# Kernel tuning notes

Hardware: AMD Instinct MI355X
Metric: run time of the kernel (lower is better)

The kernel has to match this reference:

```python
import jax, jax.numpy as jnp
from jax import lax
import numpy as np

KS = 3          # kernel_size
PAD = 1         # padding of conv_offset
N = KS * KS     # sampling points per pixel
B, C, H, W = 8, 64, 96, 96
OUTC = 64


def setup_inputs() -> dict:
    key = jax.random.key(0)
    k1, k2, k3 = jax.random.split(key, 3)
    x = jax.random.normal(k1, (B, C, H, W), dtype=jnp.float32)
    # conv_offset: Conv2d(C, 2N, ks=3, pad=1); small init so offsets are modest
    w_off = jax.random.normal(k2, (2 * N, C, KS, KS), dtype=jnp.float32) * 0.01
    b_off = jnp.zeros((2 * N,), jnp.float32)
    # conv_kernel: Conv2d(C, OUTC, ks=3, stride=3)
    w_ker = jax.random.normal(k3, (OUTC, C, KS, KS), dtype=jnp.float32) * (1.0 / np.sqrt(C * KS * KS))
    b_ker = jnp.zeros((OUTC,), jnp.float32)
    return {"x": x, "w_off": w_off, "b_off": b_off, "w_ker": w_ker, "b_ker": b_ker}


def _deform_conv(x, w_off, b_off, w_ker, b_ker):
    b, c, h, w = x.shape
    dn = ('NCHW', 'OIHW', 'NCHW')
    # offset field: (b, 2N, h, w); channels [:N] are x(row) offsets, [N:] are y(col)
    offset = lax.conv_general_dilated(x, w_off, (1, 1), [(PAD, PAD), (PAD, PAD)],
                                      dimension_numbers=dn) + b_off[None, :, None, None]
    r = jnp.arange(-(KS - 1) // 2, (KS - 1) // 2 + 1)
    pnx, pny = jnp.meshgrid(r, r, indexing='ij')          # kernel grid offsets p_n
    gx, gy = jnp.meshgrid(jnp.arange(h), jnp.arange(w), indexing='ij')  # p_0
    px = gx[None, None].astype(x.dtype) + pnx.reshape(1, N, 1, 1).astype(x.dtype) + offset[:, :N]
    py = gy[None, None].astype(x.dtype) + pny.reshape(1, N, 1, 1).astype(x.dtype) + offset[:, N:]
    # Bilinear sampling with zero outside the grid. This is exactly the dense
    # G @ x of the original (only the 4 neighbors of p have nonzero G weight).
    x0 = jnp.floor(px); y0 = jnp.floor(py)
    lx = px - x0; ly = py - y0            # grads flow to offsets through lx/ly
    x0i = lax.stop_gradient(x0).astype(jnp.int32)
    y0i = lax.stop_gradient(y0).astype(jnp.int32)
    x_flat = x.transpose(0, 2, 3, 1).reshape(b, h * w, c)  # (b, HW, c)

    def corner(xi, yi, wt):
        valid = ((xi >= 0) & (xi < h) & (yi >= 0) & (yi < w)).astype(x.dtype)
        idx = (jnp.clip(xi, 0, h - 1) * w + jnp.clip(yi, 0, w - 1)).reshape(b, -1)
        g = jax.vmap(lambda im, ix: im[ix])(x_flat, idx)   # (b, N*h*w, c)
        return g * (wt * valid).reshape(b, -1, 1)

    val = (corner(x0i,     y0i,     (1 - lx) * (1 - ly))
           + corner(x0i + 1, y0i,     lx * (1 - ly))
           + corner(x0i,     y0i + 1, (1 - lx) * ly)
           + corner(x0i + 1, y0i + 1, lx * ly))            # (b, N*h*w, c)
    xo = val.reshape(b, N, h, w, c).transpose(0, 4, 2, 3, 1)        # (b,c,h,w,N)
    # _reshape_x_offset: N -> (kr,kc) tiled into (h*ks, w*ks)
    xo = xo.reshape(b, c, h, w, KS, KS).transpose(0, 1, 2, 4, 3, 5).reshape(b, c, h * KS, w * KS)
    out = lax.conv_general_dilated(xo, w_ker, (KS, KS), 'VALID',
                                   dimension_numbers=dn) + b_ker[None, :, None, None]
    return out  # (b, OUTC, h, w)


def reference(x, w_off, b_off, w_ker, b_ker):
    return _deform_conv(x, w_off, b_off, w_ker, b_ker)
```

## Files before the change

kernel.cpp:

```cpp
#include <hip/hip_runtime.h>

#define H_ 96
#define W_ 96
#define HW 9216
#define C_ 64
#define OUTC 64
#define NPTS 9
#define NCH 18
#define B_ 8

#define PCH 72

typedef __attribute__((ext_vector_type(8))) short short8;
typedef __attribute__((ext_vector_type(4))) float f32x4;
typedef __attribute__((ext_vector_type(4))) unsigned int uint4v;

__device__ __forceinline__ short f2bf(float f) {
    union { float f; unsigned u; } v; v.f = f;
    unsigned r = v.u + 0x7fffu + ((v.u >> 16) & 1u);
    return (short)(r >> 16);
}
__device__ __forceinline__ float bflo(unsigned d) {
    union { unsigned u; float f; } v; v.u = d << 16; return v.f;
}
__device__ __forceinline__ float bfhi(unsigned d) {
    union { unsigned u; float f; } v; v.u = d & 0xffff0000u; return v.f;
}

__global__ __launch_bounds__(256) void prep_xpose(
    const float* __restrict__ x, const float* __restrict__ w_ker,
    const float* __restrict__ w_off, short* __restrict__ x_t,
    short* __restrict__ wk_frag, short* __restrict__ woff_frag)
{
    int blk = blockIdx.x;
    int t   = threadIdx.x;
    if (blk < 576) {
        int b   = blk & 7;
        int sub = blk >> 3;
        int cb  = t & 7;
        int px  = sub * 128 + (t >> 3) * 4;

        const float* xp = x + ((size_t)(b * C_ + cb * 8) * HW) + px;
        f32x4 tl[8];
#pragma unroll
        for (int e = 0; e < 8; ++e) tl[e] = *(const f32x4*)(xp + (size_t)e * HW);
#pragma unroll
        for (int p = 0; p < 4; ++p) {
            short8 s;
#pragma unroll
            for (int e = 0; e < 8; ++e) s[e] = f2bf(tl[e][p]);
            *(short8*)(x_t + ((size_t)(b * HW + px + p) * 64) + cb * 8) = s;
        }
    } else {
        int idx = (blk - 576) * 256 + t;
        if (idx < 36864) {
            int j = idx & 7, l = (idx >> 3) & 63, nt = (idx >> 9) & 3, sg = idx >> 11;
            int q2 = sg & 1, n = sg >> 1;
            int c  = q2 * 32 + ((l >> 4) << 3) + j;
            int oc = nt * 16 + (l & 15);
            wk_frag[idx] = f2bf(w_ker[(oc * C_ + c) * 9 + n]);
        } else {
            int k = idx - 36864;
            int j = k & 7, l = (k >> 3) & 63, nt = (k >> 9) & 1, sg = k >> 10;
            int q2 = sg & 1, n = sg >> 1;
            int c  = q2 * 32 + ((l >> 4) << 3) + j;
            int oc = nt * 16 + (l & 15);
            woff_frag[k] = (oc < NCH) ? f2bf(w_off[(oc * C_ + c) * 9 + n]) : (short)0;
        }
    }
}

__global__ __launch_bounds__(256, 5) void deform_fused(
    const short* __restrict__ x_t, const short* __restrict__ woff_frag,
    const float* __restrict__ b_off, const short* __restrict__ wk_frag,
    const float* __restrict__ b_ker, float* __restrict__ out)
{
    __shared__ __align__(16) short sX[160 * PCH];
    __shared__ float2 sP[4][16][9];

    int t    = threadIdx.x;
    int lane = t & 63;
    int wv   = t >> 6;
    int b    = blockIdx.x & 7;
    int s    = blockIdx.x >> 3;
    int rg   = s / 6;
    int cs   = s - rg * 6;
    int i0   = rg * 4;
    int j0   = cs * 16;
    int pxl  = lane & 15, kq = lane >> 4;
    int iw   = i0 + wv;
    int j    = j0 + pxl;
    const short* xb = x_t + (size_t)b * HW * 64;
    const short8 Z8 = {0,0,0,0,0,0,0,0};

#pragma unroll
    for (int k = 0; k < 5; ++k) {
        int u  = t + k * 256;
        int cb = u & 7, rc = u >> 3;
        int r = rc / 20, c = rc - r * 20;
        int row = min(max(i0 - 2 + r, 0), H_ - 1);
        int col = min(max(j0 - 2 + c, 0), W_ - 1);
        *(short8*)&sX[rc * PCH + cb * 8] =
            *(const short8*)(xb + (row * W_ + col) * 64 + cb * 8);
    }
    __syncthreads();

    f32x4 pa0 = {0,0,0,0}, pa1 = {0,0,0,0};
#pragma unroll
    for (int n = 0; n < 9; ++n) {
        int di = n / 3 - 1, dj = n % 3 - 1;
        bool ok = ((unsigned)(iw + di) < (unsigned)H_) & ((unsigned)(j + dj) < (unsigned)W_);
        int rcb = ((wv + di + 2) * 20 + (pxl + dj + 2)) * PCH;
#pragma unroll
        for (int q2 = 0; q2 < 2; ++q2) {
            short8 a = *(const short8*)&sX[rcb + q2 * 32 + kq * 8];
            a = ok ? a : Z8;
            const short* wb = woff_frag + ((n * 2 + q2) * 2) * 512 + lane * 8;
            short8 b0 = *(const short8*)(wb);
            short8 b1 = *(const short8*)(wb + 512);
            pa0 = __builtin_amdgcn_mfma_f32_16x16x32_bf16(a, b0, pa0, 0, 0, 0);
            pa1 = __builtin_amdgcn_mfma_f32_16x16x32_bf16(a, b1, pa1, 0, 0, 0);
        }
    }
    {
        int col = lane & 15, rq = lane >> 4;
        float bo = b_off[col];
        if (col < 9) {
#pragma unroll
            for (int r = 0; r < 4; ++r) sP[wv][rq * 4 + r][col].x = pa0[r] + bo;
        } else {
#pragma unroll
            for (int r = 0; r < 4; ++r) sP[wv][rq * 4 + r][col - 9].y = pa0[r] + bo;
        }
        if (col < 2) {
            float bo2 = b_off[16 + col];
#pragma unroll
            for (int r = 0; r < 4; ++r) sP[wv][rq * 4 + r][7 + col].y = pa1[r] + bo2;
        }
    }

    f32x4 acc[4];
#pragma unroll
    for (int nt = 0; nt < 4; ++nt) acc[nt] = (f32x4){0.f, 0.f, 0.f, 0.f};

#pragma unroll
    for (int n = 0; n < 9; ++n) {
        int di = n / 3 - 1, dj = n % 3 - 1;
        float2 o = sP[wv][pxl][n];
        float fpx = (float)(iw + di) + o.x;
        float fpy = (float)(j + dj) + o.y;
        float x0f = floorf(fpx), y0f = floorf(fpy);
        float lx = fpx - x0f, ly = fpy - y0f;
        int xi = (int)x0f, yi = (int)y0f;
        float wx0 = (xi >= 0  && xi <= H_ - 1) ? (1.0f - lx) : 0.0f;
        float wx1 = (xi >= -1 && xi <= H_ - 2) ? lx          : 0.0f;
        float wy0 = (yi >= 0  && yi <= W_ - 1) ? (1.0f - ly) : 0.0f;
        float wy1 = (yi >= -1 && yi <= W_ - 2) ? ly          : 0.0f;
        float w00 = wx0 * wy0, w10 = wx1 * wy0, w01 = wx0 * wy1, w11 = wx1 * wy1;
        int rp = xi - (i0 - 2), cp = yi - (j0 - 2);
        bool inp = (rp >= 0) & (rp <= 6) & (cp >= 0) & (cp <= 18);
        uint4v u[8];
        if (inp) {
            int l00 = (rp * 20 + cp) * PCH;
            int l10 = l00 + 20 * PCH, l01 = l00 + PCH, l11 = l10 + PCH;
#pragma unroll
            for (int q2 = 0; q2 < 2; ++q2) {
                int cho = q2 * 32 + kq * 8;
                u[q2*4+0] = *(const uint4v*)&sX[l00 + cho];
                u[q2*4+1] = *(const uint4v*)&sX[l10 + cho];
                u[q2*4+2] = *(const uint4v*)&sX[l01 + cho];
                u[q2*4+3] = *(const uint4v*)&sX[l11 + cho];
            }
        }
        if (!inp) {
            int r0 = min(max(xi,     0), H_ - 1) * W_;
            int r1 = min(max(xi + 1, 0), H_ - 1) * W_;
            int c0 = min(max(yi,     0), W_ - 1);
            int c1 = min(max(yi + 1, 0), W_ - 1);
#pragma unroll
            for (int q2 = 0; q2 < 2; ++q2) {
                int cho = q2 * 32 + kq * 8;
                u[q2*4+0] = *(const uint4v*)(xb + (r0 + c0) * 64 + cho);
                u[q2*4+1] = *(const uint4v*)(xb + (r1 + c0) * 64 + cho);
                u[q2*4+2] = *(const uint4v*)(xb + (r0 + c1) * 64 + cho);
                u[q2*4+3] = *(const uint4v*)(xb + (r1 + c1) * 64 + cho);
            }
        }
#pragma unroll
        for (int q2 = 0; q2 < 2; ++q2) {
            short8 A;
#pragma unroll
            for (int d = 0; d < 4; ++d) {
                float lo = w00 * bflo(u[q2*4+0][d]) + w10 * bflo(u[q2*4+1][d])
                         + w01 * bflo(u[q2*4+2][d]) + w11 * bflo(u[q2*4+3][d]);
                float hi = w00 * bfhi(u[q2*4+0][d]) + w10 * bfhi(u[q2*4+1][d])
                         + w01 * bfhi(u[q2*4+2][d]) + w11 * bfhi(u[q2*4+3][d]);
                A[2 * d]     = f2bf(lo);
                A[2 * d + 1] = f2bf(hi);
            }
            const short* wbp = wk_frag + ((n * 2 + q2) * 4) * 512 + lane * 8;
#pragma unroll
            for (int nt = 0; nt < 4; ++nt) {
                short8 bfr = *(const short8*)(wbp + nt * 512);
                acc[nt] = __builtin_amdgcn_mfma_f32_16x16x32_bf16(A, bfr, acc[nt], 0, 0, 0);
            }
        }
    }

    __syncthreads();
    float* fw = (float*)sX + wv * 1280;
    {
        int col = lane & 15, rq = lane >> 4;
#pragma unroll
        for (int nt = 0; nt < 4; ++nt) {
            int oc = nt * 16 + col;
            float bias = b_ker[oc];
#pragma unroll
            for (int r = 0; r < 4; ++r)
                fw[oc * 20 + rq * 4 + r] = acc[nt][r] + bias;
        }
    }
    {
        int ocl = lane >> 2, qq = lane & 3;
        float* ob = out + (size_t)b * OUTC * HW + iw * W_ + j0 + qq * 4;
#pragma unroll
        for (int it = 0; it < 4; ++it) {
            int oc = it * 16 + ocl;
            f32x4 v = *(const f32x4*)&fw[oc * 20 + qq * 4];
            *(f32x4*)(ob + (size_t)oc * HW) = v;
        }
    }
}

extern "C" void kernel_launch(void* const* d_in, const int* in_sizes, int n_in,
                              void* d_out, int out_size, void* d_ws, size_t ws_size,
                              hipStream_t stream) {
    const float* x     = (const float*)d_in[0];
    const float* w_off = (const float*)d_in[1];
    const float* b_off = (const float*)d_in[2];
    const float* w_ker = (const float*)d_in[3];
    const float* b_ker = (const float*)d_in[4];
    float* out = (float*)d_out;

    char*  wsb       = (char*)d_ws;
    short* x_t       = (short*)wsb;
    short* wk_frag   = (short*)(wsb + 9437184);
    short* woff_frag = wk_frag + 36864;

    prep_xpose  <<<792,  256, 0, stream>>>(x, w_ker, w_off, x_t, wk_frag, woff_frag);
    deform_fused<<<1152, 256, 0, stream>>>(x_t, woff_frag, b_off, wk_frag, b_ker, out);
}
```

Before: 105.9 us.

## Drop NHWC bf16 transpose pass; load NCHW fp32 tiles directly into shared memory

Measured after the change: 108.4 us. 2.4% more time.

```diff
diff --git a/kernel.cpp b/kernel.cpp
--- a/kernel.cpp
+++ b/kernel.cpp
@@ -9,17 +9,22 @@
 #define NCH 18
 #define B_ 8
 
+#define PW  24
 #define PCH 72
 
 typedef __attribute__((ext_vector_type(8))) short short8;
 typedef __attribute__((ext_vector_type(4))) float f32x4;
 typedef __attribute__((ext_vector_type(4))) unsigned int uint4v;
+typedef __attribute__((ext_vector_type(2))) unsigned int uint2v;
 
 __device__ __forceinline__ short f2bf(float f) {
     union { float f; unsigned u; } v; v.f = f;
     unsigned r = v.u + 0x7fffu + ((v.u >> 16) & 1u);
     return (short)(r >> 16);
 }
+__device__ __forceinline__ unsigned pk2bf(float lo, float hi) {
+    return ((unsigned)(unsigned short)f2bf(hi) << 16) | (unsigned short)f2bf(lo);
+}
 __device__ __forceinline__ float bflo(unsigned d) {
     union { unsigned u; float f; } v; v.u = d << 16; return v.f;
 }
@@ -27,55 +32,33 @@
     union { unsigned u; float f; } v; v.u = d & 0xffff0000u; return v.f;
 }
 
-__global__ __launch_bounds__(256) void prep_xpose(
-    const float* __restrict__ x, const float* __restrict__ w_ker,
-    const float* __restrict__ w_off, short* __restrict__ x_t,
+__global__ __launch_bounds__(256) void prep_w(
+    const float* __restrict__ w_ker, const float* __restrict__ w_off,
     short* __restrict__ wk_frag, short* __restrict__ woff_frag)
 {
-    int blk = blockIdx.x;
-    int t   = threadIdx.x;
-    if (blk < 576) {
-        int b   = blk & 7;
-        int sub = blk >> 3;
-        int cb  = t & 7;
-        int px  = sub * 128 + (t >> 3) * 4;
-
-        const float* xp = x + ((size_t)(b * C_ + cb * 8) * HW) + px;
-        f32x4 tl[8];
-#pragma unroll
-        for (int e = 0; e < 8; ++e) tl[e] = *(const f32x4*)(xp + (size_t)e * HW);
-#pragma unroll
-        for (int p = 0; p < 4; ++p) {
-            short8 s;
-#pragma unroll
-            for (int e = 0; e < 8; ++e) s[e] = f2bf(tl[e][p]);
-            *(short8*)(x_t + ((size_t)(b * HW + px + p) * 64) + cb * 8) = s;
-        }
+    int idx = blockIdx.x * 256 + threadIdx.x;
+    if (idx < 36864) {
+        int j = idx & 7, l = (idx >> 3) & 63, nt = (idx >> 9) & 3, sg = idx >> 11;
+        int q2 = sg & 1, n = sg >> 1;
+        int c  = q2 * 32 + ((l >> 4) << 3) + j;
+        int oc = nt * 16 + (l & 15);
+        wk_frag[idx] = f2bf(w_ker[(oc * C_ + c) * 9 + n]);
     } else {
-        int idx = (blk - 576) * 256 + t;
-        if (idx < 36864) {
-            int j = idx & 7, l = (idx >> 3) & 63, nt = (idx >> 9) & 3, sg = idx >> 11;
-            int q2 = sg & 1, n = sg >> 1;
-            int c  = q2 * 32 + ((l >> 4) << 3) + j;
-            int oc = nt * 16 + (l & 15);
-            wk_frag[idx] = f2bf(w_ker[(oc * C_ + c) * 9 + n]);
-        } else {
-            int k = idx - 36864;
-            int j = k & 7, l = (k >> 3) & 63, nt = (k >> 9) & 1, sg = k >> 10;
-            int q2 = sg & 1, n = sg >> 1;
-            int c  = q2 * 32 + ((l >> 4) << 3) + j;
-            int oc = nt * 16 + (l & 15);
-            woff_frag[k] = (oc < NCH) ? f2bf(w_off[(oc * C_ + c) * 9 + n]) : (short)0;
-        }
+        int k = idx - 36864;
+        int j = k & 7, l = (k >> 3) & 63, nt = (k >> 9) & 1, sg = k >> 10;
+        int q2 = sg & 1, n = sg >> 1;
+        int c  = q2 * 32 + ((l >> 4) << 3) + j;
+        int oc = nt * 16 + (l & 15);
+        woff_frag[k] = (oc < NCH) ? f2bf(w_off[(oc * C_ + c) * 9 + n]) : (short)0;
     }
 }
 
 __global__ __launch_bounds__(256, 5) void deform_fused(
-    const short* __restrict__ x_t, const short* __restrict__ woff_frag,
+    const float* __restrict__ x, const short* __restrict__ woff_frag,
     const float* __restrict__ b_off, const short* __restrict__ wk_frag,
     const float* __restrict__ b_ker, float* __restrict__ out)
 {
-    __shared__ __align__(16) short sX[160 * PCH];
+    __shared__ __align__(16) short sX[192 * PCH];
     __shared__ float2 sP[4][16][9];
 
     int t    = threadIdx.x;
@@ -90,18 +73,39 @@
     int pxl  = lane & 15, kq = lane >> 4;
     int iw   = i0 + wv;
     int j    = j0 + pxl;
-    const short* xb = x_t + (size_t)b * HW * 64;
+    const float* xb = x + (size_t)b * C_ * HW;
     const short8 Z8 = {0,0,0,0,0,0,0,0};
 
 #pragma unroll
-    for (int k = 0; k < 5; ++k) {
-        int u  = t + k * 256;
-        int cb = u & 7, rc = u >> 3;
-        int r = rc / 20, c = rc - r * 20;
+    for (int k = 0; k < 3; ++k) {
+        int u   = t + k * 256;
+        int q   = u % 6;
+        int rem = u / 6;
+        int r   = rem & 7;
+        int cq  = rem >> 3;
         int row = min(max(i0 - 2 + r, 0), H_ - 1);
-        int col = min(max(j0 - 2 + c, 0), W_ - 1);
-        *(short8*)&sX[rc * PCH + cb * 8] =
-            *(const short8*)(xb + (row * W_ + col) * 64 + cb * 8);
+        int c0  = j0 - 4 + q * 4;
+        const float* pb = xb + (size_t)(4 * cq) * HW + row * W_;
+        f32x4 v[4];
+        if (c0 >= 0 && c0 <= W_ - 4) {
+#pragma unroll
+            for (int e = 0; e < 4; ++e) v[e] = *(const f32x4*)(pb + (size_t)e * HW + c0);
+        } else {
+#pragma unroll
+            for (int p = 0; p < 4; ++p) {
+                int cc = min(max(c0 + p, 0), W_ - 1);
+#pragma unroll
+                for (int e = 0; e < 4; ++e) v[e][p] = pb[(size_t)e * HW + cc];
+            }
+        }
+        int sbase = (r * PW + q * 4) * PCH + 4 * cq;
+#pragma unroll
+        for (int p = 0; p < 4; ++p) {
+            uint2v w;
+            w[0] = pk2bf(v[0][p], v[1][p]);
+            w[1] = pk2bf(v[2][p], v[3][p]);
+            *(uint2v*)&sX[sbase + p * PCH] = w;
+        }
     }
     __syncthreads();
 
@@ -110,7 +114,7 @@
     for (int n = 0; n < 9; ++n) {
         int di = n / 3 - 1, dj = n % 3 - 1;
         bool ok = ((unsigned)(iw + di) < (unsigned)H_) & ((unsigned)(j + dj) < (unsigned)W_);
-        int rcb = ((wv + di + 2) * 20 + (pxl + dj + 2)) * PCH;
+        int rcb = ((wv + di + 2) * PW + (pxl + dj + 4)) * PCH;
 #pragma unroll
         for (int q2 = 0; q2 < 2; ++q2) {
             short8 a = *(const short8*)&sX[rcb + q2 * 32 + kq * 8];
@@ -157,12 +161,12 @@
         float wy0 = (yi >= 0  && yi <= W_ - 1) ? (1.0f - ly) : 0.0f;
         float wy1 = (yi >= -1 && yi <= W_ - 2) ? ly          : 0.0f;
         float w00 = wx0 * wy0, w10 = wx1 * wy0, w01 = wx0 * wy1, w11 = wx1 * wy1;
-        int rp = xi - (i0 - 2), cp = yi - (j0 - 2);
-        bool inp = (rp >= 0) & (rp <= 6) & (cp >= 0) & (cp <= 18);
+        int rp = xi - (i0 - 2), cp = yi - (j0 - 4);
+        bool inp = (rp >= 0) & (rp <= 6) & (cp >= 0) & (cp <= 22);
         uint4v u[8];
         if (inp) {
-            int l00 = (rp * 20 + cp) * PCH;
-            int l10 = l00 + 20 * PCH, l01 = l00 + PCH, l11 = l10 + PCH;
+            int l00 = (rp * PW + cp) * PCH;
+            int l10 = l00 + PW * PCH, l01 = l00 + PCH, l11 = l10 + PCH;
 #pragma unroll
             for (int q2 = 0; q2 < 2; ++q2) {
                 int cho = q2 * 32 + kq * 8;
@@ -180,10 +184,16 @@
 #pragma unroll
             for (int q2 = 0; q2 < 2; ++q2) {
                 int cho = q2 * 32 + kq * 8;
-                u[q2*4+0] = *(const uint4v*)(xb + (r0 + c0) * 64 + cho);
-                u[q2*4+1] = *(const uint4v*)(xb + (r1 + c0) * 64 + cho);
-                u[q2*4+2] = *(const uint4v*)(xb + (r0 + c1) * 64 + cho);
-                u[q2*4+3] = *(const uint4v*)(xb + (r1 + c1) * 64 + cho);
+                const float* xc = xb + (size_t)cho * HW;
+#pragma unroll
+                for (int d = 0; d < 4; ++d) {
+                    const float* p0 = xc + (size_t)(2 * d) * HW;
+                    const float* p1 = p0 + HW;
+                    u[q2*4+0][d] = pk2bf(p0[r0 + c0], p1[r0 + c0]);
+                    u[q2*4+1][d] = pk2bf(p0[r1 + c0], p1[r1 + c0]);
+                    u[q2*4+2][d] = pk2bf(p0[r0 + c1], p1[r0 + c1]);
+                    u[q2*4+3][d] = pk2bf(p0[r1 + c1], p1[r1 + c1]);
+                }
             }
         }
 #pragma unroll
@@ -243,10 +253,9 @@
     float* out = (float*)d_out;
 
     char*  wsb       = (char*)d_ws;
-    short* x_t       = (short*)wsb;
-    short* wk_frag   = (short*)(wsb + 9437184);
+    short* wk_frag   = (short*)wsb;
     short* woff_frag = wk_frag + 36864;
 
-    prep_xpose  <<<792,  256, 0, stream>>>(x, w_ker, w_off, x_t, wk_frag, woff_frag);
-    deform_fused<<<1152, 256, 0, stream>>>(x_t, woff_frag, b_off, wk_frag, b_ker, out);
-}
+    prep_w      <<<216,  256, 0, stream>>>(w_ker, w_off, wk_frag, woff_frag);
+    deform_fused<<<1152, 256, 0, stream>>>(x, woff_frag, b_off, wk_frag, b_ker, out);
+}
```
